# Performance work log

Measured on AMD Instinct MI355X. Metric: run time of the kernel, lower is better.

The kernel has to match this reference:

```python
import jax, jax.numpy as jnp
import numpy as np

ALPHA = 1.0  # self.alpha_ in ClusterNet


def setup_inputs() -> dict:
    key = jax.random.key(0)
    k1, k2 = jax.random.split(key)
    z = jax.random.normal(k1, (8192, 256), dtype=jnp.float32)
    centroids = jax.random.normal(k2, (64, 256), dtype=jnp.float32)
    return {"z": z, "centroids": centroids}


def reference(z, centroids):
    # similarity='EUC': pairwise euclidean distance (bs, n_clusters)
    diff = z[:, None, :] - centroids[None, :, :]          # (bs, K, H)
    sim = jnp.sqrt(jnp.sum(diff * diff, axis=2))          # (bs, K)
    # Student-t soft assignment, alpha = 1 -> Q = (1 + sim)^-1
    Q = jnp.power(1.0 + sim / ALPHA, -(ALPHA + 1.0) / 2.0)
    Q = Q / jnp.sum(Q, axis=1, keepdims=True)             # row-normalize
    # Target distribution P
    P = jnp.square(Q) / jnp.sum(Q, axis=0, keepdims=True)  # col-sum of Q
    P = P / jnp.sum(P, axis=1, keepdims=True)              # row-normalize
    return (Q, P)
```

## Files before the change

kernel.cpp:

```cpp
#include <hip/hip_runtime.h>


#define M  8192
#define NC 64
#define H  256
#define BM 16

__global__ __launch_bounds__(512, 4) void k1_fused(
    const float* __restrict__ Z, const float* __restrict__ C,
    float* __restrict__ out, float* __restrict__ ws)
{
    __shared__ float pd[8][BM][NC];
    __shared__ float ncp[8][NC];
    __shared__ float nzs[BM];
    __shared__ float csum[8][NC];

    const int t    = threadIdx.x;
    const int lane = t & 63;
    const int wid  = __builtin_amdgcn_readfirstlane(t >> 6);
    const int row0 = blockIdx.x * BM;

    {
        const int r  = t >> 5;
        const int sg = t & 31;
        const float4* zr = (const float4*)(Z + (size_t)(row0 + r) * H);
        float s = 0.f;
        #pragma unroll
        for (int i = 0; i < 2; ++i) {
            float4 v = zr[sg * 2 + i];
            s += v.x * v.x + v.y * v.y + v.z * v.z + v.w * v.w;
        }
        s += __shfl_xor(s, 1);
        s += __shfl_xor(s, 2);
        s += __shfl_xor(s, 4);
        s += __shfl_xor(s, 8);
        s += __shfl_xor(s, 16);
        if (sg == 0) nzs[r] = s;
    }

    float4 c4[8];
    {
        const float4* cp = (const float4*)(C + (size_t)lane * H + wid * 32);
        #pragma unroll
        for (int i = 0; i < 8; ++i) c4[i] = cp[i];
    }
    {
        float s = 0.f;
        #pragma unroll
        for (int i = 0; i < 8; ++i)
            s += c4[i].x * c4[i].x + c4[i].y * c4[i].y + c4[i].z * c4[i].z + c4[i].w * c4[i].w;
        ncp[wid][lane] = s;
    }

    float acc[BM];
    #pragma unroll
    for (int r = 0; r < BM; ++r) acc[r] = 0.f;

    const float* Zb = Z + (size_t)row0 * H + wid * 32;
    #pragma unroll
    for (int kb = 0; kb < 2; ++kb) {
        #pragma unroll
        for (int r = 0; r < BM; ++r) {
            const float4* zp = (const float4*)(Zb + r * H + kb * 16);
            float4 z0 = zp[0], z1 = zp[1], z2 = zp[2], z3 = zp[3];
            float a = acc[r];
            a += z0.x * c4[kb*4+0].x + z0.y * c4[kb*4+0].y + z0.z * c4[kb*4+0].z + z0.w * c4[kb*4+0].w;
            a += z1.x * c4[kb*4+1].x + z1.y * c4[kb*4+1].y + z1.z * c4[kb*4+1].z + z1.w * c4[kb*4+1].w;
            a += z2.x * c4[kb*4+2].x + z2.y * c4[kb*4+2].y + z2.z * c4[kb*4+2].z + z2.w * c4[kb*4+2].w;
            a += z3.x * c4[kb*4+3].x + z3.y * c4[kb*4+3].y + z3.z * c4[kb*4+3].z + z3.w * c4[kb*4+3].w;
            acc[r] = a;
        }
    }

    #pragma unroll
    for (int r = 0; r < BM; ++r) pd[wid][r][lane] = acc[r];
    __syncthreads();

    const float ncT = ncp[0][lane] + ncp[1][lane] + ncp[2][lane] + ncp[3][lane]
                    + ncp[4][lane] + ncp[5][lane] + ncp[6][lane] + ncp[7][lane];
    float colLocal = 0.f;
    #pragma unroll
    for (int j = 0; j < 2; ++j) {
        const int r = wid * 2 + j;
        float dot = pd[0][r][lane] + pd[1][r][lane] + pd[2][r][lane] + pd[3][r][lane]
                  + pd[4][r][lane] + pd[5][r][lane] + pd[6][r][lane] + pd[7][r][lane];
        float d2  = fmaxf(nzs[r] + ncT - 2.f * dot, 0.f);
        float q   = 1.f / (1.f + sqrtf(d2));
        float s = q;
        s += __shfl_xor(s, 1);
        s += __shfl_xor(s, 2);
        s += __shfl_xor(s, 4);
        s += __shfl_xor(s, 8);
        s += __shfl_xor(s, 16);
        s += __shfl_xor(s, 32);
        float qn = q / s;
        out[(size_t)(row0 + r) * NC + lane] = qn;
        colLocal += qn;
    }
    csum[wid][lane] = colLocal;
    __syncthreads();
    if (wid == 0)
        ws[blockIdx.x * NC + lane] =
            csum[0][lane] + csum[1][lane] + csum[2][lane] + csum[3][lane] +
            csum[4][lane] + csum[5][lane] + csum[6][lane] + csum[7][lane];
}

__global__ __launch_bounds__(256, 2) void k2_p(
    float* __restrict__ out, const float* __restrict__ ws)
{
    __shared__ float4 red[256];
    __shared__ float invcs[NC];
    const int t  = threadIdx.x;
    const int g  = t & 15;
    const int s0 = t >> 4;
    const float4* w4 = (const float4*)ws;
    float4 a = make_float4(0.f, 0.f, 0.f, 0.f);
    #pragma unroll
    for (int i = 0; i < 32; ++i) {
        float4 v = w4[(size_t)(s0 + 16 * i) * 16 + g];
        a.x += v.x; a.y += v.y; a.z += v.z; a.w += v.w;
    }
    red[t] = a;
    __syncthreads();
    if (t < 16) {
        float4 s = red[t];
        for (int i = 1; i < 16; ++i) {
            float4 v = red[i * 16 + t];
            s.x += v.x; s.y += v.y; s.z += v.z; s.w += v.w;
        }
        invcs[4 * t + 0] = 1.f / s.x;
        invcs[4 * t + 1] = 1.f / s.y;
        invcs[4 * t + 2] = 1.f / s.z;
        invcs[4 * t + 3] = 1.f / s.w;
    }
    __syncthreads();

    const int lane = t & 63;
    const int wid  = t >> 6;
    const float ic = invcs[lane];
    const int row0 = blockIdx.x * BM;
    #pragma unroll
    for (int j = 0; j < 4; ++j) {
        const int r = row0 + wid * 4 + j;
        float q  = out[(size_t)r * NC + lane];
        float pr = q * q * ic;
        float s = pr;
        s += __shfl_xor(s, 1);
        s += __shfl_xor(s, 2);
        s += __shfl_xor(s, 4);
        s += __shfl_xor(s, 8);
        s += __shfl_xor(s, 16);
        s += __shfl_xor(s, 32);
        out[(size_t)(M + r) * NC + lane] = pr / s;
    }
}

extern "C" void kernel_launch(void* const* d_in, const int* in_sizes, int n_in,
                              void* d_out, int out_size, void* d_ws, size_t ws_size,
                              hipStream_t stream) {
    const float* Z = (const float*)d_in[0];
    const float* C = (const float*)d_in[1];
    float* out = (float*)d_out;
    float* ws  = (float*)d_ws;

    k1_fused<<<512, 512, 0, stream>>>(Z, C, out, ws);
    k2_p<<<512, 256, 0, stream>>>(out, ws);
}
```

Baseline: 73.31 us.

## Fuse Q and P kernels into one using grid-wide flag synchronization

Merges the two kernels into a single launch. Each block publishes its column-sum partials and sets a flag. The first 8 blocks spin on those flags, reduce the column sums and publish inverse totals through a second set of flags; every block then waits for those and computes P from Q values still held in registers. This removes the second launch and the re-read of Q from global memory, but it depends on all 512 blocks being resident at once. The flags are never reset, so on repeated calls the waits can pass early and read stale values.

```diff
diff --git a/kernel.cpp b/kernel.cpp
--- a/kernel.cpp
+++ b/kernel.cpp
@@ -5,20 +5,32 @@
 #define NC 64
 #define H  256
 #define BM 16
+#define NBLK 512
+#define MAGIC 0x13579BDFu
 
-__global__ __launch_bounds__(512, 4) void k1_fused(
+
+__global__ __launch_bounds__(512, 4) void k_fused(
     const float* __restrict__ Z, const float* __restrict__ C,
-    float* __restrict__ out, float* __restrict__ ws)
+    float* __restrict__ out, float* __restrict__ wsf)
 {
     __shared__ float pd[8][BM][NC];
     __shared__ float ncp[8][NC];
     __shared__ float nzs[BM];
     __shared__ float csum[8][NC];
+    __shared__ float red[NBLK];
+    __shared__ float invl[NC];
+
+    unsigned int* wsu = (unsigned int*)wsf;
+    float* partials      = wsf;
+    unsigned int* aflag  = wsu + 32768;
+    unsigned int* rflag  = wsu + 33344;
+    float* invg          = wsf + 33408;
 
     const int t    = threadIdx.x;
     const int lane = t & 63;
     const int wid  = __builtin_amdgcn_readfirstlane(t >> 6);
-    const int row0 = blockIdx.x * BM;
+    const int bid  = blockIdx.x;
+    const int row0 = bid * BM;
 
     {
         const int r  = t >> 5;
@@ -78,6 +90,7 @@
 
     const float ncT = ncp[0][lane] + ncp[1][lane] + ncp[2][lane] + ncp[3][lane]
                     + ncp[4][lane] + ncp[5][lane] + ncp[6][lane] + ncp[7][lane];
+    float qreg[2];
     float colLocal = 0.f;
     #pragma unroll
     for (int j = 0; j < 2; ++j) {
@@ -95,55 +108,60 @@
         s += __shfl_xor(s, 32);
         float qn = q / s;
         out[(size_t)(row0 + r) * NC + lane] = qn;
+        qreg[j] = qn;
         colLocal += qn;
     }
     csum[wid][lane] = colLocal;
     __syncthreads();
+
     if (wid == 0)
-        ws[blockIdx.x * NC + lane] =
+        partials[bid * NC + lane] =
             csum[0][lane] + csum[1][lane] + csum[2][lane] + csum[3][lane] +
             csum[4][lane] + csum[5][lane] + csum[6][lane] + csum[7][lane];
-}
+    __threadfence();
+    __syncthreads();
+    if (t == 0)
+        __hip_atomic_store(&aflag[bid], MAGIC, __ATOMIC_RELAXED, __HIP_MEMORY_SCOPE_AGENT);
 
-__global__ __launch_bounds__(256, 2) void k2_p(
-    float* __restrict__ out, const float* __restrict__ ws)
-{
-    __shared__ float4 red[256];
-    __shared__ float invcs[NC];
-    const int t  = threadIdx.x;
-    const int g  = t & 15;
-    const int s0 = t >> 4;
-    const float4* w4 = (const float4*)ws;
-    float4 a = make_float4(0.f, 0.f, 0.f, 0.f);
-    #pragma unroll
-    for (int i = 0; i < 32; ++i) {
-        float4 v = w4[(size_t)(s0 + 16 * i) * 16 + g];
-        a.x += v.x; a.y += v.y; a.z += v.z; a.w += v.w;
+    if (bid < 8) {
+        while (__hip_atomic_load(&aflag[t], __ATOMIC_RELAXED, __HIP_MEMORY_SCOPE_AGENT) != MAGIC)
+            __builtin_amdgcn_s_sleep(1);
+        __threadfence();
+        __syncthreads();
+        const int c  = bid * 8 + (t & 7);
+        const int i0 = t >> 3;
+        float s = 0.f;
+        #pragma unroll
+        for (int k = 0; k < 8; ++k)
+            s += partials[(i0 + 64 * k) * NC + c];
+        red[t] = s;
+        __syncthreads();
+        if (t < 8) {
+            float tot = 0.f;
+            for (int i = 0; i < 64; ++i) tot += red[i * 8 + t];
+            __hip_atomic_store(&invg[bid * 8 + t], 1.f / tot,
+                               __ATOMIC_RELAXED, __HIP_MEMORY_SCOPE_AGENT);
+        }
+        __threadfence();
+        __syncthreads();
+        if (t == 0)
+            __hip_atomic_store(&rflag[bid], MAGIC, __ATOMIC_RELAXED, __HIP_MEMORY_SCOPE_AGENT);
     }
-    red[t] = a;
+
+    if (t < 8)
+        while (__hip_atomic_load(&rflag[t], __ATOMIC_RELAXED, __HIP_MEMORY_SCOPE_AGENT) != MAGIC)
+            __builtin_amdgcn_s_sleep(2);
+    __threadfence();
     __syncthreads();
-    if (t < 16) {
-        float4 s = red[t];
-        for (int i = 1; i < 16; ++i) {
-            float4 v = red[i * 16 + t];
-            s.x += v.x; s.y += v.y; s.z += v.z; s.w += v.w;
-        }
-        invcs[4 * t + 0] = 1.f / s.x;
-        invcs[4 * t + 1] = 1.f / s.y;
-        invcs[4 * t + 2] = 1.f / s.z;
-        invcs[4 * t + 3] = 1.f / s.w;
-    }
+    if (t < NC)
+        invl[t] = __hip_atomic_load(&invg[t], __ATOMIC_RELAXED, __HIP_MEMORY_SCOPE_AGENT);
     __syncthreads();
 
-    const int lane = t & 63;
-    const int wid  = t >> 6;
-    const float ic = invcs[lane];
-    const int row0 = blockIdx.x * BM;
+    const float ic = invl[lane];
     #pragma unroll
-    for (int j = 0; j < 4; ++j) {
-        const int r = row0 + wid * 4 + j;
-        float q  = out[(size_t)r * NC + lane];
-        float pr = q * q * ic;
+    for (int j = 0; j < 2; ++j) {
+        const int r = wid * 2 + j;
+        float pr = qreg[j] * qreg[j] * ic;
         float s = pr;
         s += __shfl_xor(s, 1);
         s += __shfl_xor(s, 2);
@@ -151,7 +169,7 @@
         s += __shfl_xor(s, 8);
         s += __shfl_xor(s, 16);
         s += __shfl_xor(s, 32);
-        out[(size_t)(M + r) * NC + lane] = pr / s;
+        out[(size_t)(M + row0 + r) * NC + lane] = pr / s;
     }
 }
 
@@ -163,6 +181,5 @@
     float* out = (float*)d_out;
     float* ws  = (float*)d_ws;
 
-    k1_fused<<<512, 512, 0, stream>>>(Z, C, out, ws);
-    k2_p<<<512, 256, 0, stream>>>(out, ws);
+    k_fused<<<NBLK, 512, 0, stream>>>(Z, C, out, ws);
 }
```

New measurement: 198.6 us. +171.0%, slower.

## Halve rows per block and hoist column-sum reduction into separate small kernel

Applied to the files above, without the earlier changes.

The distance/Q kernel now handles 8 rows per block across 1024 blocks with a higher occupancy hint, so more blocks run concurrently. The column-sum reduction that every P-block used to repeat is moved into a dedicated 16-block kernel that writes inverse column sums once, and the P kernel just reads them. This removes 512 redundant reductions over the workspace but adds a third kernel launch and an extra dependency step. Each block in the first kernel now does half the work on the same centroid register load, so centroid reloads per row double.

```diff
diff --git a/kernel.cpp b/kernel.cpp
--- a/kernel.cpp
+++ b/kernel.cpp
@@ -1,12 +1,15 @@
 #include <hip/hip_runtime.h>
 
 
-#define M  8192
-#define NC 64
-#define H  256
-#define BM 16
+#define M   8192
+#define NC  64
+#define H   256
+#define BM  8
+#define NB1 1024
+#define BM2 16
 
-__global__ __launch_bounds__(512, 4) void k1_fused(
+
+__global__ __launch_bounds__(512, 8) void k1_dist_q(
     const float* __restrict__ Z, const float* __restrict__ C,
     float* __restrict__ out, float* __restrict__ ws)
 {
@@ -21,21 +24,15 @@
     const int row0 = blockIdx.x * BM;
 
     {
-        const int r  = t >> 5;
-        const int sg = t & 31;
-        const float4* zr = (const float4*)(Z + (size_t)(row0 + r) * H);
-        float s = 0.f;
-        #pragma unroll
-        for (int i = 0; i < 2; ++i) {
-            float4 v = zr[sg * 2 + i];
-            s += v.x * v.x + v.y * v.y + v.z * v.z + v.w * v.w;
-        }
+        float4 v = ((const float4*)(Z + (size_t)(row0 + wid) * H))[lane];
+        float s = v.x * v.x + v.y * v.y + v.z * v.z + v.w * v.w;
         s += __shfl_xor(s, 1);
         s += __shfl_xor(s, 2);
         s += __shfl_xor(s, 4);
         s += __shfl_xor(s, 8);
         s += __shfl_xor(s, 16);
-        if (sg == 0) nzs[r] = s;
+        s += __shfl_xor(s, 32);
+        if (lane == 0) nzs[wid] = s;
     }
 
     float4 c4[8];
@@ -78,10 +75,8 @@
 
     const float ncT = ncp[0][lane] + ncp[1][lane] + ncp[2][lane] + ncp[3][lane]
                     + ncp[4][lane] + ncp[5][lane] + ncp[6][lane] + ncp[7][lane];
-    float colLocal = 0.f;
-    #pragma unroll
-    for (int j = 0; j < 2; ++j) {
-        const int r = wid * 2 + j;
+    {
+        const int r = wid;
         float dot = pd[0][r][lane] + pd[1][r][lane] + pd[2][r][lane] + pd[3][r][lane]
                   + pd[4][r][lane] + pd[5][r][lane] + pd[6][r][lane] + pd[7][r][lane];
         float d2  = fmaxf(nzs[r] + ncT - 2.f * dot, 0.f);
@@ -95,9 +90,8 @@
         s += __shfl_xor(s, 32);
         float qn = q / s;
         out[(size_t)(row0 + r) * NC + lane] = qn;
-        colLocal += qn;
+        csum[wid][lane] = qn;
     }
-    csum[wid][lane] = colLocal;
     __syncthreads();
     if (wid == 0)
         ws[blockIdx.x * NC + lane] =
@@ -105,40 +99,34 @@
             csum[4][lane] + csum[5][lane] + csum[6][lane] + csum[7][lane];
 }
 
+__global__ __launch_bounds__(256, 2) void kmid_reduce(
+    const float* __restrict__ ws, float* __restrict__ invcs)
+{
+    __shared__ float red[256];
+    const int t = threadIdx.x;
+    const int c = blockIdx.x * 4 + (t & 3);
+    const int r0 = t >> 2;
+    float s = 0.f;
+    #pragma unroll
+    for (int j = 0; j < 16; ++j)
+        s += ws[(size_t)(r0 + 64 * j) * NC + c];
+    red[t] = s;
+    __syncthreads();
+    if (t < 4) {
+        float tot = 0.f;
+        for (int g = 0; g < 64; ++g) tot += red[g * 4 + t];
+        invcs[blockIdx.x * 4 + t] = 1.f / tot;
+    }
+}
+
 __global__ __launch_bounds__(256, 2) void k2_p(
-    float* __restrict__ out, const float* __restrict__ ws)
+    float* __restrict__ out, const float* __restrict__ invcs)
 {
-    __shared__ float4 red[256];
-    __shared__ float invcs[NC];
-    const int t  = threadIdx.x;
-    const int g  = t & 15;
-    const int s0 = t >> 4;
-    const float4* w4 = (const float4*)ws;
-    float4 a = make_float4(0.f, 0.f, 0.f, 0.f);
-    #pragma unroll
-    for (int i = 0; i < 32; ++i) {
-        float4 v = w4[(size_t)(s0 + 16 * i) * 16 + g];
-        a.x += v.x; a.y += v.y; a.z += v.z; a.w += v.w;
-    }
-    red[t] = a;
-    __syncthreads();
-    if (t < 16) {
-        float4 s = red[t];
-        for (int i = 1; i < 16; ++i) {
-            float4 v = red[i * 16 + t];
-            s.x += v.x; s.y += v.y; s.z += v.z; s.w += v.w;
-        }
-        invcs[4 * t + 0] = 1.f / s.x;
-        invcs[4 * t + 1] = 1.f / s.y;
-        invcs[4 * t + 2] = 1.f / s.z;
-        invcs[4 * t + 3] = 1.f / s.w;
-    }
-    __syncthreads();
-
+    const int t    = threadIdx.x;
     const int lane = t & 63;
     const int wid  = t >> 6;
     const float ic = invcs[lane];
-    const int row0 = blockIdx.x * BM;
+    const int row0 = blockIdx.x * BM2;
     #pragma unroll
     for (int j = 0; j < 4; ++j) {
         const int r = row0 + wid * 4 + j;
@@ -162,7 +150,9 @@
     const float* C = (const float*)d_in[1];
     float* out = (float*)d_out;
     float* ws  = (float*)d_ws;
+    float* invcs = ws + 65536;
 
-    k1_fused<<<512, 512, 0, stream>>>(Z, C, out, ws);
-    k2_p<<<512, 256, 0, stream>>>(out, ws);
+    k1_dist_q<<<NB1, 512, 0, stream>>>(Z, C, out, ws);
+    kmid_reduce<<<16, 256, 0, stream>>>(ws, invcs);
+    k2_p<<<512, 256, 0, stream>>>(out, invcs);
 }
```

Measured after the change: 74.45 us. Within noise of the previous version (+1.6%).
